# Kernel tuning notes

Measured on AMD Instinct MI355X. Metric: run time of the kernel, lower is better.

The kernel has to match this reference:

```python
import jax, jax.numpy as jnp
import numpy as np

B, S, E, H = 2, 2048, 1024, 16
D = E // H  # head dim = 64
NEG_INF = -1e30


def alibi_slopes(n_head):
    # standard ALiBi slopes: 2^(-8*i/n_head), i = 1..n_head
    return jnp.asarray([2.0 ** (-8.0 * (i + 1) / n_head) for i in range(n_head)], dtype=jnp.float32)


def setup_inputs() -> dict:
    key = jax.random.key(0)
    ks = jax.random.split(key, 5)
    scale = 0.02
    return {
        "x": jax.random.normal(ks[0], (B, S, E), dtype=jnp.float32),
        "W_kqv": jax.random.normal(ks[1], (E, 3 * E), dtype=jnp.float32) * scale,
        "b_kqv": jnp.zeros((3 * E,), dtype=jnp.float32),
        "W_proj": jax.random.normal(ks[2], (E, E), dtype=jnp.float32) * scale,
        "b_proj": jnp.zeros((E,), dtype=jnp.float32),
        "slopes": alibi_slopes(H),
    }


def reference(x, W_kqv, b_kqv, W_proj, b_proj, slopes):
    b, s, e = x.shape
    kqv = x @ W_kqv + b_kqv                       # [b, s, 3e]
    k, q, v = jnp.split(kqv, 3, axis=-1)          # split order: k, q, v
    k = k.reshape(b, s, H, D)
    q = q.reshape(b, s, H, D)
    v = v.reshape(b, s, H, D)
    attn = jnp.einsum("bqhd,bkhd->bhqk", q, k) * (1.0 / jnp.sqrt(jnp.float32(D)))
    # ALiBi bias: slope_h * (j - i) for j <= i, -inf above diagonal (causal)
    i = jnp.arange(s)[:, None]
    j = jnp.arange(s)[None, :]
    rel = (j - i).astype(jnp.float32)             # [s, s]
    bias = slopes[:, None, None] * jnp.tril(rel)  # [h, s, s]
    bias = jnp.where(j > i, NEG_INF, bias)
    attn = jax.nn.softmax(attn + bias[None], axis=-1)
    # dropout is identity in eval mode
    y = jnp.einsum("bhqk,bkhd->bqhd", attn, v).reshape(b, s, e)
    return y @ W_proj + b_proj
```

## Files before the change

kernel.cpp:

```cpp
#include <hip/hip_runtime.h>

typedef unsigned short u16;
typedef float f32x4 __attribute__((ext_vector_type(4)));
typedef __bf16 bfx8 __attribute__((ext_vector_type(8)));
typedef __bf16 bfx4 __attribute__((ext_vector_type(4)));
typedef u16 u16x8 __attribute__((ext_vector_type(8)));
typedef u16 u16x4 __attribute__((ext_vector_type(4)));

#define B_ 2
#define S_ 2048
#define E_ 1024
#define H_ 16
#define D_ 64

__device__ __forceinline__ u16 f2bf(float f) {
  unsigned u = __float_as_uint(f);
  u = u + 0x7FFFu + ((u >> 16) & 1u);
  return (u16)(u >> 16);
}

__device__ __forceinline__ int swz128(int o) { return o ^ ((o >> 3) & 0x70); }

__device__ __forceinline__ void gload16(const void* g, void* l) {
  __builtin_amdgcn_global_load_lds((const __attribute__((address_space(1))) void*)g,
                                   (__attribute__((address_space(3))) void*)l, 16, 0, 0);
}

__global__ __launch_bounds__(256) void prep(const float* __restrict__ x,
                                            const float* __restrict__ Wk,
                                            const float* __restrict__ Wp, u16* __restrict__ xb,
                                            u16* __restrict__ wkt, u16* __restrict__ wpt) {
  __shared__ float tile[64][65];
  const int id = blockIdx.x, tid = threadIdx.x;
  if (id < 2048) {
    const float4* in4 = reinterpret_cast<const float4*>(x);
    u16x4* out4 = reinterpret_cast<u16x4*>(xb);
    int i = id * 256 + tid;
#pragma unroll
    for (int p = 0; p < 2; ++p, i += 524288) {
      const float4 v = in4[i];
      u16x4 o = {f2bf(v.x), f2bf(v.y), f2bf(v.z), f2bf(v.w)};
      out4[i] = o;
    }
    return;
  }
  const float* in;
  u16* out;
  int R, C, bx, by;
  if (id < 2816) {
    const int t = id - 2048;
    in = Wk; out = wkt; R = 1024; C = 3072; bx = t % 48; by = t / 48;
  } else {
    const int t = id - 2816;
    in = Wp; out = wpt; R = 1024; C = 1024; bx = t & 15; by = t >> 4;
  }
  const int ct = bx * 64, rt = by * 64;
#pragma unroll
  for (int p = 0; p < 4; ++p) {
    int f = p * 256 + tid;
    int row = f >> 4, c4 = (f & 15) << 2;
    const float4 v = *reinterpret_cast<const float4*>(in + (size_t)(rt + row) * C + ct + c4);
    tile[row][c4 + 0] = v.x; tile[row][c4 + 1] = v.y;
    tile[row][c4 + 2] = v.z; tile[row][c4 + 3] = v.w;
  }
  __syncthreads();
#pragma unroll
  for (int p = 0; p < 4; ++p) {
    int g = p * 256 + tid;
    int orow = g >> 4, k4 = (g & 15) << 2;
    u16x4 o = {f2bf(tile[k4 + 0][orow]), f2bf(tile[k4 + 1][orow]),
               f2bf(tile[k4 + 2][orow]), f2bf(tile[k4 + 3][orow])};
    *reinterpret_cast<u16x4*>(out + (size_t)(ct + orow) * R + rt + k4) = o;
  }
}

template <int EPI>
__global__ __launch_bounds__(256) void gemm_bt(const u16* __restrict__ A,
                                               const u16* __restrict__ Bt,
                                               const float* __restrict__ bias, int M, int N, int K,
                                               float* __restrict__ outF, u16* __restrict__ outK,
                                               u16* __restrict__ outQ, u16* __restrict__ outVt) {
  __shared__ __align__(16) u16 sA[128 * 64];
  __shared__ __align__(16) u16 sB[128 * 64];
  const int tid = threadIdx.x, lane = tid & 63;
  const int wave = tid >> 6, wr = wave >> 1, wc = wave & 1;
  int lin = blockIdx.y * gridDim.x + blockIdx.x;
  const int nwg = gridDim.x * gridDim.y;
  if ((nwg & 7) == 0) {
    const int cpx = nwg >> 3;
    lin = (lin & 7) * cpx + (lin >> 3);
  }
  const int bm = (lin / gridDim.x) * 128, bn = (lin % gridDim.x) * 128;
  const int r8 = lane >> 3, c16 = (lane & 7) ^ r8;
  f32x4 acc[4][4] = {};
  for (int k0 = 0; k0 < K; k0 += 64) {
#pragma unroll
    for (int i = 0; i < 4; ++i) {
      const int c = wave * 4 + i;
      const int row = c * 8 + r8;
      gload16(A + (size_t)(bm + row) * K + k0 + c16 * 8, (char*)sA + c * 1024);
      gload16(Bt + (size_t)(bn + row) * K + k0 + c16 * 8, (char*)sB + c * 1024);
    }
    __syncthreads();
#pragma unroll
    for (int kc = 0; kc < 2; ++kc) {
      bfx8 af[4], bf[4];
#pragma unroll
      for (int mf = 0; mf < 4; ++mf) {
        int o = swz128(((wr * 64 + mf * 16 + (lane & 15)) << 7) + kc * 64 + ((lane >> 4) << 4));
        af[mf] = *reinterpret_cast<const bfx8*>(reinterpret_cast<const char*>(sA) + o);
      }
#pragma unroll
      for (int nf = 0; nf < 4; ++nf) {
        int o = swz128(((wc * 64 + nf * 16 + (lane & 15)) << 7) + kc * 64 + ((lane >> 4) << 4));
        bf[nf] = *reinterpret_cast<const bfx8*>(reinterpret_cast<const char*>(sB) + o);
      }
#pragma unroll
      for (int mf = 0; mf < 4; ++mf)
#pragma unroll
        for (int nf = 0; nf < 4; ++nf)
          acc[mf][nf] = __builtin_amdgcn_mfma_f32_16x16x32_bf16(af[mf], bf[nf], acc[mf][nf], 0, 0, 0);
    }
    __syncthreads();
  }
#pragma unroll
  for (int mf = 0; mf < 4; ++mf)
#pragma unroll
    for (int nf = 0; nf < 4; ++nf)
#pragma unroll
      for (int r = 0; r < 4; ++r) {
        const int row = bm + wr * 64 + mf * 16 + ((lane >> 4) << 2) + r;
        const int col = bn + wc * 64 + nf * 16 + (lane & 15);
        const float v = acc[mf][nf][r] + bias[col];
        if (EPI == 1) {
          outF[(size_t)row * N + col] = v;
        } else {
          const int chunk = col >> 10, w = col & 1023, h = w >> 6, dd = w & 63;
          const int b = row >> 11, s = row & 2047;
          const int bh = b * H_ + h;
          if (chunk == 0)
            outK[((size_t)bh * S_ + s) * D_ + dd] = f2bf(v);
          else if (chunk == 1)
            outQ[((size_t)bh * S_ + s) * D_ + dd] = f2bf(v);
          else
            outVt[((size_t)bh * D_ + dd) * S_ + s] = f2bf(v);
        }
      }
}

__global__ __launch_bounds__(256, 4) void attn_alibi(const u16* __restrict__ Q,
                                                     const u16* __restrict__ Kb,
                                                     const u16* __restrict__ Vt,
                                                     const float* __restrict__ slopes,
                                                     u16* __restrict__ Y) {
  __shared__ __align__(16) u16 sK[2][4096];
  __shared__ __align__(16) u16 sV[2][4096];
  __shared__ __align__(16) __bf16 sP[4][16 * 64];
  const int id = blockIdx.x;
  const int hi2 = id >> 8, rem = id & 255;
  const int r5 = rem & 31;
  const int qi = (hi2 & 1) ? r5 : 31 - r5;
  const int bh = (hi2 << 3) + (rem >> 5);
  const int b = bh >> 4, h = bh & 15;
  const int tid = threadIdx.x, lane = tid & 63, wave = tid >> 6;
  const int q = lane & 15, g = lane >> 4;
  const int q0 = qi * 64;
  const int w0 = q0 + wave * 16;
  const float L2E = 1.44269504089f;
  const float SCALE = 0.125f * L2E;
  const float sl2 = slopes[h] * L2E;
  const size_t headSD = (size_t)bh * (S_ * D_);
  const size_t headDS = (size_t)bh * (D_ * S_);
  const int nt = qi + 1;
  const int r8 = lane >> 3, c16 = (lane & 7) ^ r8;

  bfx8 qf[2];
  {
    const u16* qp = Q + headSD + (size_t)(w0 + q) * D_ + g * 8;
    qf[0] = *reinterpret_cast<const bfx8*>(qp);
    qf[1] = *reinterpret_cast<const bfx8*>(qp + 32);
  }
  f32x4 base[4];
#pragma unroll
  for (int nf = 0; nf < 4; ++nf)
#pragma unroll
    for (int r = 0; r < 4; ++r) base[nf][r] = sl2 * (float)(nf * 16 + 4 * g + r);
  const int ir0 = wave * 16 + q;

  float m = 0.f, l = 0.f;
  f32x4 oT[4] = {};

  auto stage = [&](int t, int buf) {
#pragma unroll
    for (int i = 0; i < 2; ++i) {
      const int c = wave * 2 + i;
      const int row = c * 8 + r8;
      gload16(Kb + headSD + (size_t)t * 4096 + row * 64 + c16 * 8, (char*)sK[buf] + c * 1024);
      gload16(Vt + headDS + (size_t)row * S_ + t * 64 + c16 * 8, (char*)sV[buf] + c * 1024);
    }
  };

  stage(0, 0);
  __syncthreads();
  int cur = 0;
  for (int t = 0; t < nt; ++t) {
    if (t + 1 < nt) stage(t + 1, cur ^ 1);
    const char* sKc = reinterpret_cast<const char*>(sK[cur]);
    const char* sVc = reinterpret_cast<const char*>(sV[cur]);
    f32x4 tt[4] = {};
#pragma unroll
    for (int kc = 0; kc < 2; ++kc)
#pragma unroll
      for (int nf = 0; nf < 4; ++nf) {
        const bfx8 kf =
            *reinterpret_cast<const bfx8*>(sKc + swz128(((nf * 16 + q) << 7) + kc * 64 + (g << 4)));
        tt[nf] = __builtin_amdgcn_mfma_f32_16x16x32_bf16(kf, qf[kc], tt[nf], 0, 0, 0);
      }
    const float tb = sl2 * (float)(t * 64);
    const bool last = (t == nt - 1);
    float rmax = -3.0e38f;
#pragma unroll
    for (int nf = 0; nf < 4; ++nf)
#pragma unroll
      for (int r = 0; r < 4; ++r) {
        float sv = fmaf(tt[nf][r], SCALE, base[nf][r] + tb);
        if (last && (nf * 16 + 4 * g + r > ir0)) sv = -3.0e38f;
        tt[nf][r] = sv;
        rmax = fmaxf(rmax, sv);
      }
    rmax = fmaxf(rmax, __shfl_xor(rmax, 16));
    rmax = fmaxf(rmax, __shfl_xor(rmax, 32));
    if (!__all(rmax <= m + 12.0f)) {
      const float mnew = fmaxf(m, rmax);
      const float corr = __builtin_amdgcn_exp2f(m - mnew);
      m = mnew;
      l *= corr;
#pragma unroll
      for (int nf = 0; nf < 4; ++nf) oT[nf] *= corr;
    }
    float rsum = 0.f;
#pragma unroll
    for (int nf = 0; nf < 4; ++nf)
#pragma unroll
      for (int r = 0; r < 4; ++r) {
        const float pe = __builtin_amdgcn_exp2f(tt[nf][r] - m);
        tt[nf][r] = pe;
        rsum += pe;
      }
    rsum += __shfl_xor(rsum, 16);
    rsum += __shfl_xor(rsum, 32);
    l += rsum;
    char* pw = reinterpret_cast<char*>(sP[wave]);
#pragma unroll
    for (int nf = 0; nf < 4; ++nf) {
      bfx4 w = {(__bf16)tt[nf][0], (__bf16)tt[nf][1], (__bf16)tt[nf][2], (__bf16)tt[nf][3]};
      *reinterpret_cast<bfx4*>(pw + swz128((q << 7) + nf * 32 + g * 8)) = w;
    }
    bfx8 pa[2];
#pragma unroll
    for (int kc = 0; kc < 2; ++kc)
      pa[kc] = *reinterpret_cast<const bfx8*>(pw + swz128((q << 7) + kc * 64 + (g << 4)));
#pragma unroll
    for (int kc = 0; kc < 2; ++kc)
#pragma unroll
      for (int nf = 0; nf < 4; ++nf) {
        const bfx8 vf =
            *reinterpret_cast<const bfx8*>(sVc + swz128(((nf * 16 + q) << 7) + kc * 64 + (g << 4)));
        oT[nf] = __builtin_amdgcn_mfma_f32_16x16x32_bf16(vf, pa[kc], oT[nf], 0, 0, 0);
      }
    __syncthreads();
    cur ^= 1;
  }
  const float rl = 1.0f / l;
  const int row = w0 + q;
#pragma unroll
  for (int nf = 0; nf < 4; ++nf) {
    bfx4 w = {(__bf16)(oT[nf][0] * rl), (__bf16)(oT[nf][1] * rl), (__bf16)(oT[nf][2] * rl),
              (__bf16)(oT[nf][3] * rl)};
    const int col = h * 64 + nf * 16 + g * 4;
    *reinterpret_cast<bfx4*>(reinterpret_cast<char*>(Y) + (((size_t)b * S_ + row) * E_ + col) * 2) =
        w;
  }
}

extern "C" void kernel_launch(void* const* d_in, const int* in_sizes, int n_in, void* d_out,
                              int out_size, void* d_ws, size_t ws_size, hipStream_t stream) {
  (void)in_sizes; (void)n_in; (void)out_size; (void)ws_size;
  const float* x = (const float*)d_in[0];
  const float* Wkqv = (const float*)d_in[1];
  const float* bkqv = (const float*)d_in[2];
  const float* Wproj = (const float*)d_in[3];
  const float* bproj = (const float*)d_in[4];
  const float* slopes = (const float*)d_in[5];
  float* out = (float*)d_out;

  const size_t MBE = (size_t)4096 * 1024;
  u16* xb = (u16*)d_ws;
  u16* wkqvt = xb + MBE;
  u16* wprojt = wkqvt + (size_t)3072 * 1024;
  u16* kbuf = wprojt + (size_t)1024 * 1024;
  u16* qbuf = kbuf + MBE;
  u16* vtbuf = qbuf + MBE;
  u16* ybuf = vtbuf + MBE;

  prep<<<dim3(3072), dim3(256), 0, stream>>>(x, Wkqv, Wproj, xb, wkqvt, wprojt);
  gemm_bt<0><<<dim3(24, 32), dim3(256), 0, stream>>>(xb, wkqvt, bkqv, 4096, 3072, 1024,
                                                     (float*)nullptr, kbuf, qbuf, vtbuf);
  attn_alibi<<<dim3(1024), dim3(256), 0, stream>>>(qbuf, kbuf, vtbuf, slopes, ybuf);
  gemm_bt<1><<<dim3(8, 32), dim3(256), 0, stream>>>(ybuf, wprojt, bproj, 4096, 1024, 1024, out,
                                                    nullptr, nullptr, nullptr);
}
```

Measured before the change: 122.5 us.

## Streamline attention softmax, compute row sums via MFMA, add 512-thread proj GEMM

For non-diagonal tiles the attention kernel now bounds the running max from the raw score max plus the largest ALiBi offset, then fuses scale, bias and exp into one FMA+exp2 per element. The row sum is computed with an extra MFMA against a ones vector instead of shuffle reductions, and s_setprio raises priority around the MFMA sections. The output projection gets its own 512-thread kernel with 8 waves each computing a 64x32 sub-tile, which gives more waves per block. The bound-based max is an overestimate, so it trades some tightness of the max for fewer reductions, and the sum now comes from bf16-rounded probabilities.

```diff
diff --git a/kernel.cpp b/kernel.cpp
--- a/kernel.cpp
+++ b/kernel.cpp
@@ -74,12 +74,11 @@
   }
 }
 
-template <int EPI>
-__global__ __launch_bounds__(256) void gemm_bt(const u16* __restrict__ A,
-                                               const u16* __restrict__ Bt,
-                                               const float* __restrict__ bias, int M, int N, int K,
-                                               float* __restrict__ outF, u16* __restrict__ outK,
-                                               u16* __restrict__ outQ, u16* __restrict__ outVt) {
+__global__ __launch_bounds__(256) void gemm_kqv(const u16* __restrict__ A,
+                                                const u16* __restrict__ Bt,
+                                                const float* __restrict__ bias, int M, int N, int K,
+                                                u16* __restrict__ outK, u16* __restrict__ outQ,
+                                                u16* __restrict__ outVt) {
   __shared__ __align__(16) u16 sA[128 * 64];
   __shared__ __align__(16) u16 sB[128 * 64];
   const int tid = threadIdx.x, lane = tid & 63;
@@ -132,19 +131,74 @@
         const int row = bm + wr * 64 + mf * 16 + ((lane >> 4) << 2) + r;
         const int col = bn + wc * 64 + nf * 16 + (lane & 15);
         const float v = acc[mf][nf][r] + bias[col];
-        if (EPI == 1) {
-          outF[(size_t)row * N + col] = v;
-        } else {
-          const int chunk = col >> 10, w = col & 1023, h = w >> 6, dd = w & 63;
-          const int b = row >> 11, s = row & 2047;
-          const int bh = b * H_ + h;
-          if (chunk == 0)
-            outK[((size_t)bh * S_ + s) * D_ + dd] = f2bf(v);
-          else if (chunk == 1)
-            outQ[((size_t)bh * S_ + s) * D_ + dd] = f2bf(v);
-          else
-            outVt[((size_t)bh * D_ + dd) * S_ + s] = f2bf(v);
-        }
+        const int chunk = col >> 10, w = col & 1023, h = w >> 6, dd = w & 63;
+        const int b = row >> 11, s = row & 2047;
+        const int bh = b * H_ + h;
+        if (chunk == 0)
+          outK[((size_t)bh * S_ + s) * D_ + dd] = f2bf(v);
+        else if (chunk == 1)
+          outQ[((size_t)bh * S_ + s) * D_ + dd] = f2bf(v);
+        else
+          outVt[((size_t)bh * D_ + dd) * S_ + s] = f2bf(v);
+      }
+}
+
+__global__ __launch_bounds__(512) void gemm_proj(const u16* __restrict__ A,
+                                                 const u16* __restrict__ Bt,
+                                                 const float* __restrict__ bias, int M, int N,
+                                                 int K, float* __restrict__ outF) {
+  __shared__ __align__(16) u16 sA[128 * 64];
+  __shared__ __align__(16) u16 sB[128 * 64];
+  const int tid = threadIdx.x, lane = tid & 63;
+  const int wave = tid >> 6, wr = wave >> 2, wc = wave & 3;
+  int lin = blockIdx.y * gridDim.x + blockIdx.x;
+  const int nwg = gridDim.x * gridDim.y;
+  if ((nwg & 7) == 0) {
+    const int cpx = nwg >> 3;
+    lin = (lin & 7) * cpx + (lin >> 3);
+  }
+  const int bm = (lin / gridDim.x) * 128, bn = (lin % gridDim.x) * 128;
+  const int r8 = lane >> 3, c16 = (lane & 7) ^ r8;
+  f32x4 acc[4][2] = {};
+  for (int k0 = 0; k0 < K; k0 += 64) {
+#pragma unroll
+    for (int i = 0; i < 2; ++i) {
+      const int c = wave * 2 + i;
+      const int row = c * 8 + r8;
+      gload16(A + (size_t)(bm + row) * K + k0 + c16 * 8, (char*)sA + c * 1024);
+      gload16(Bt + (size_t)(bn + row) * K + k0 + c16 * 8, (char*)sB + c * 1024);
+    }
+    __syncthreads();
+#pragma unroll
+    for (int kc = 0; kc < 2; ++kc) {
+      bfx8 af[4], bf[2];
+#pragma unroll
+      for (int mf = 0; mf < 4; ++mf) {
+        int o = swz128(((wr * 64 + mf * 16 + (lane & 15)) << 7) + kc * 64 + ((lane >> 4) << 4));
+        af[mf] = *reinterpret_cast<const bfx8*>(reinterpret_cast<const char*>(sA) + o);
+      }
+#pragma unroll
+      for (int nf = 0; nf < 2; ++nf) {
+        int o = swz128(((wc * 32 + nf * 16 + (lane & 15)) << 7) + kc * 64 + ((lane >> 4) << 4));
+        bf[nf] = *reinterpret_cast<const bfx8*>(reinterpret_cast<const char*>(sB) + o);
+      }
+#pragma unroll
+      for (int mf = 0; mf < 4; ++mf)
+#pragma unroll
+        for (int nf = 0; nf < 2; ++nf)
+          acc[mf][nf] = __builtin_amdgcn_mfma_f32_16x16x32_bf16(af[mf], bf[nf], acc[mf][nf], 0, 0, 0);
+    }
+    __syncthreads();
+  }
+#pragma unroll
+  for (int mf = 0; mf < 4; ++mf)
+#pragma unroll
+    for (int nf = 0; nf < 2; ++nf)
+#pragma unroll
+      for (int r = 0; r < 4; ++r) {
+        const int row = bm + wr * 64 + mf * 16 + ((lane >> 4) << 2) + r;
+        const int col = bn + wc * 32 + nf * 16 + (lane & 15);
+        outF[(size_t)row * N + col] = acc[mf][nf][r] + bias[col];
       }
 }
 
@@ -180,6 +234,9 @@
     qf[0] = *reinterpret_cast<const bfx8*>(qp);
     qf[1] = *reinterpret_cast<const bfx8*>(qp + 32);
   }
+  bfx8 onesf;
+#pragma unroll
+  for (int j = 0; j < 8; ++j) onesf[j] = (__bf16)1.0f;
   f32x4 base[4];
 #pragma unroll
   for (int nf = 0; nf < 4; ++nf)
@@ -187,8 +244,9 @@
     for (int r = 0; r < 4; ++r) base[nf][r] = sl2 * (float)(nf * 16 + 4 * g + r);
   const int ir0 = wave * 16 + q;
 
-  float m = 0.f, l = 0.f;
+  float m = 0.f;
   f32x4 oT[4] = {};
+  f32x4 oX = {};
 
   auto stage = [&](int t, int buf) {
 #pragma unroll
@@ -208,6 +266,7 @@
     const char* sKc = reinterpret_cast<const char*>(sK[cur]);
     const char* sVc = reinterpret_cast<const char*>(sV[cur]);
     f32x4 tt[4] = {};
+    __builtin_amdgcn_s_setprio(1);
 #pragma unroll
     for (int kc = 0; kc < 2; ++kc)
 #pragma unroll
@@ -216,40 +275,59 @@
             *reinterpret_cast<const bfx8*>(sKc + swz128(((nf * 16 + q) << 7) + kc * 64 + (g << 4)));
         tt[nf] = __builtin_amdgcn_mfma_f32_16x16x32_bf16(kf, qf[kc], tt[nf], 0, 0, 0);
       }
+    __builtin_amdgcn_s_setprio(0);
     const float tb = sl2 * (float)(t * 64);
-    const bool last = (t == nt - 1);
-    float rmax = -3.0e38f;
-#pragma unroll
-    for (int nf = 0; nf < 4; ++nf)
-#pragma unroll
-      for (int r = 0; r < 4; ++r) {
-        float sv = fmaf(tt[nf][r], SCALE, base[nf][r] + tb);
-        if (last && (nf * 16 + 4 * g + r > ir0)) sv = -3.0e38f;
-        tt[nf][r] = sv;
-        rmax = fmaxf(rmax, sv);
-      }
-    rmax = fmaxf(rmax, __shfl_xor(rmax, 16));
-    rmax = fmaxf(rmax, __shfl_xor(rmax, 32));
-    if (!__all(rmax <= m + 12.0f)) {
-      const float mnew = fmaxf(m, rmax);
-      const float corr = __builtin_amdgcn_exp2f(m - mnew);
-      m = mnew;
-      l *= corr;
-#pragma unroll
-      for (int nf = 0; nf < 4; ++nf) oT[nf] *= corr;
-    }
-    float rsum = 0.f;
-#pragma unroll
-    for (int nf = 0; nf < 4; ++nf)
-#pragma unroll
-      for (int r = 0; r < 4; ++r) {
-        const float pe = __builtin_amdgcn_exp2f(tt[nf][r] - m);
-        tt[nf][r] = pe;
-        rsum += pe;
-      }
-    rsum += __shfl_xor(rsum, 16);
-    rsum += __shfl_xor(rsum, 32);
-    l += rsum;
+    if (t != nt - 1) {
+      float rmax = -3.0e38f;
+#pragma unroll
+      for (int nf = 0; nf < 4; ++nf)
+#pragma unroll
+        for (int r = 0; r < 4; ++r) rmax = fmaxf(rmax, tt[nf][r]);
+      rmax = fmaxf(rmax, __shfl_xor(rmax, 16));
+      rmax = fmaxf(rmax, __shfl_xor(rmax, 32));
+      const float bound = fmaf(rmax, SCALE, tb + sl2 * 63.f);
+      if (!__all(bound <= m + 12.0f)) {
+        const float mnew = fmaxf(m, bound);
+        const float corr = __builtin_amdgcn_exp2f(m - mnew);
+        m = mnew;
+#pragma unroll
+        for (int nf = 0; nf < 4; ++nf) oT[nf] *= corr;
+        oX *= corr;
+      }
+      const float tbm = tb - m;
+#pragma unroll
+      for (int nf = 0; nf < 4; ++nf) {
+        const f32x4 bb = base[nf] + tbm;
+#pragma unroll
+        for (int r = 0; r < 4; ++r)
+          tt[nf][r] = __builtin_amdgcn_exp2f(fmaf(tt[nf][r], SCALE, bb[r]));
+      }
+    } else {
+      float rmax = -3.0e38f;
+#pragma unroll
+      for (int nf = 0; nf < 4; ++nf)
+#pragma unroll
+        for (int r = 0; r < 4; ++r) {
+          float sv = fmaf(tt[nf][r], SCALE, base[nf][r] + tb);
+          if (nf * 16 + 4 * g + r > ir0) sv = -3.0e38f;
+          tt[nf][r] = sv;
+          rmax = fmaxf(rmax, sv);
+        }
+      rmax = fmaxf(rmax, __shfl_xor(rmax, 16));
+      rmax = fmaxf(rmax, __shfl_xor(rmax, 32));
+      if (!__all(rmax <= m + 12.0f)) {
+        const float mnew = fmaxf(m, rmax);
+        const float corr = __builtin_amdgcn_exp2f(m - mnew);
+        m = mnew;
+#pragma unroll
+        for (int nf = 0; nf < 4; ++nf) oT[nf] *= corr;
+        oX *= corr;
+      }
+#pragma unroll
+      for (int nf = 0; nf < 4; ++nf)
+#pragma unroll
+        for (int r = 0; r < 4; ++r) tt[nf][r] = __builtin_amdgcn_exp2f(tt[nf][r] - m);
+    }
     char* pw = reinterpret_cast<char*>(sP[wave]);
 #pragma unroll
     for (int nf = 0; nf < 4; ++nf) {
@@ -260,18 +338,22 @@
 #pragma unroll
     for (int kc = 0; kc < 2; ++kc)
       pa[kc] = *reinterpret_cast<const bfx8*>(pw + swz128((q << 7) + kc * 64 + (g << 4)));
-#pragma unroll
-    for (int kc = 0; kc < 2; ++kc)
+    __builtin_amdgcn_s_setprio(1);
+#pragma unroll
+    for (int kc = 0; kc < 2; ++kc) {
 #pragma unroll
       for (int nf = 0; nf < 4; ++nf) {
         const bfx8 vf =
             *reinterpret_cast<const bfx8*>(sVc + swz128(((nf * 16 + q) << 7) + kc * 64 + (g << 4)));
         oT[nf] = __builtin_amdgcn_mfma_f32_16x16x32_bf16(vf, pa[kc], oT[nf], 0, 0, 0);
       }
+      oX = __builtin_amdgcn_mfma_f32_16x16x32_bf16(onesf, pa[kc], oX, 0, 0, 0);
+    }
+    __builtin_amdgcn_s_setprio(0);
     __syncthreads();
     cur ^= 1;
   }
-  const float rl = 1.0f / l;
+  const float rl = 1.0f / oX[0];
   const int row = w0 + q;
 #pragma unroll
   for (int nf = 0; nf < 4; ++nf) {
@@ -304,9 +386,8 @@
   u16* ybuf = vtbuf + MBE;
 
   prep<<<dim3(3072), dim3(256), 0, stream>>>(x, Wkqv, Wproj, xb, wkqvt, wprojt);
-  gemm_bt<0><<<dim3(24, 32), dim3(256), 0, stream>>>(xb, wkqvt, bkqv, 4096, 3072, 1024,
-                                                     (float*)nullptr, kbuf, qbuf, vtbuf);
+  gemm_kqv<<<dim3(24, 32), dim3(256), 0, stream>>>(xb, wkqvt, bkqv, 4096, 3072, 1024, kbuf, qbuf,
+                                                   vtbuf);
   attn_alibi<<<dim3(1024), dim3(256), 0, stream>>>(qbuf, kbuf, vtbuf, slopes, ybuf);
-  gemm_bt<1><<<dim3(8, 32), dim3(256), 0, stream>>>(ybuf, wprojt, bproj, 4096, 1024, 1024, out,
-                                                    nullptr, nullptr, nullptr);
-}
+  gemm_proj<<<dim3(8, 32), dim3(512), 0, stream>>>(ybuf, wprojt, bproj, 4096, 1024, 1024, out);
+}
```

New measurement: 118.9 us. -2.9%, faster.
